# Kernel tuning notes

Hardware: AMD Instinct MI355X
Metric: run time of the kernel (lower is better)

Reference implementation:

```python
import jax, jax.numpy as jnp
import numpy as np

EPS = 1e-6
H, A, V = 4, 64, 64  # heads, attn_dim, hidden_dim


def layer_norm(x, w, b):
    mu = jnp.mean(x, axis=-1, keepdims=True)
    var = jnp.var(x, axis=-1, keepdims=True)
    return (x - mu) * jax.lax.rsqrt(var + EPS) * w + b


def setup_inputs() -> dict:
    key = jax.random.key(0)
    B, N, D = 4, 2048, 512
    lengths = np.array([2048, 1536, 1024, 1792], np.int32)
    offsets = np.concatenate([[0], np.cumsum(lengths)]).astype(np.int32)
    L = int(offsets[-1])  # 6400
    uvqk_out = (2 * V + 2 * A) * H  # 1024
    out_in = 2 * V * H + D          # concat([u, x, normed_attn])
    ks = jax.random.split(key, 4)
    return {
        "x": jax.random.normal(ks[0], (L, D), jnp.float32),
        "x_lengths": jnp.asarray(lengths),
        "x_offsets": jnp.asarray(offsets),
        "max_seq_len": N,
        "num_targets": jnp.asarray([32, 16, 8, 64], jnp.int32),
        "uvqk_weight": jax.random.normal(ks[1], (D, uvqk_out), jnp.float32) / np.float32(np.sqrt(D)),
        "uvqk_bias": jnp.zeros((uvqk_out,), jnp.float32),
        "input_norm_weight": jnp.ones((D,), jnp.float32),
        "input_norm_bias": jnp.zeros((D,), jnp.float32),
        "output_norm_weight": jnp.ones((V * H,), jnp.float32),
        "output_norm_bias": jnp.zeros((V * H,), jnp.float32),
        "output_weight": jax.random.normal(ks[2], (out_in, D), jnp.float32) / np.float32(np.sqrt(out_in)),
    }


def reference(x, x_lengths, x_offsets, max_seq_len, num_targets,
              uvqk_weight, uvqk_bias, input_norm_weight, input_norm_bias,
              output_norm_weight, output_norm_bias, output_weight):
    L, D = x.shape
    B = x_lengths.shape[0]
    N = int(max_seq_len)
    alpha = A ** -0.5

    # fused input layernorm + UVQK projection + silu
    nx = layer_norm(x, input_norm_weight, input_norm_bias)
    uvqk = jax.nn.silu(nx @ uvqk_weight + uvqk_bias)              # [L, (2V+2A)*H]
    u = uvqk[:, : V * H]                                          # [L, V*H]
    v = uvqk[:, V * H: 2 * V * H].reshape(L, H, V)
    q = uvqk[:, 2 * V * H: 2 * V * H + A * H].reshape(L, H, A)
    k = uvqk[:, 2 * V * H + A * H:].reshape(L, H, A)

    # jagged -> padded [B, N, ...]
    pos = jnp.arange(N)
    gather_idx = jnp.clip(x_offsets[:-1, None] + pos[None, :], 0, L - 1)  # [B,N]
    valid = pos[None, :] < x_lengths[:, None]                              # [B,N]
    qp = q[gather_idx] * valid[..., None, None]
    kp = k[gather_idx] * valid[..., None, None]
    vp = v[gather_idx] * valid[..., None, None]

    # target-aware causal mask: clamp ids at uih boundary; eye | dist>0
    max_ids = (x_lengths - num_targets)[:, None]        # [B,1]
    ids = jnp.minimum(pos[None, :], max_ids)            # [B,N]
    dist = ids[:, :, None] - ids[:, None, :]            # [B,N,N]
    mask = (dist > 0) | jnp.eye(N, dtype=bool)[None]
    mask = mask & valid[:, :, None] & valid[:, None, :]

    scores = jnp.einsum("bnha,bmha->bhnm", qp, kp) * alpha
    attn_w = jax.nn.silu(scores) * (1.0 / N)
    attn_w = attn_w * mask[:, None].astype(attn_w.dtype)
    attn_p = jnp.einsum("bhnm,bmhv->bnhv", attn_w, vp).reshape(B, N, H * V)

    # padded -> jagged
    tok = jnp.arange(L)
    b_of = jnp.searchsorted(x_offsets, tok, side="right") - 1
    p_of = tok - x_offsets[b_of]
    attn = attn_p[b_of, p_of]                            # [L, H*V]

    # output: norm(attn), concat [u, x, y], project, residual (dropout off / eval)
    y = layer_norm(attn, output_norm_weight, output_norm_bias)
    y = jnp.concatenate([u, x, y], axis=1)
    return x + y @ output_weight
```

## Files before the change

### kernel.cpp

```cpp
#include <hip/hip_runtime.h>
#include <math.h>

#define NSEQ 2048
#define PIT 72

typedef __attribute__((ext_vector_type(8))) short short8;
typedef __attribute__((ext_vector_type(4))) short short4v;
typedef __attribute__((ext_vector_type(4))) float f32x4;

__device__ __forceinline__ float silu_f(float z) {
    return z * __builtin_amdgcn_rcpf(1.f + __expf(-z));
}

__device__ __forceinline__ unsigned short f2bf(float f) {
    unsigned int u = __float_as_uint(f);
    u += 0x7fffu + ((u >> 16) & 1u);
    return (unsigned short)(u >> 16);
}

__device__ __forceinline__ unsigned short f2bf_fast(float f) {
    return (unsigned short)((__float_as_uint(f) + 0x8000u) >> 16);
}

__device__ __forceinline__ short8 scale8_pow2(short8 v, float s) {
    short8 r;
    #pragma unroll
    for (int i = 0; i < 8; i++) {
        float f = __uint_as_float(((unsigned int)(unsigned short)v[i]) << 16) * s;
        r[i] = (short)(unsigned short)(__float_as_uint(f) >> 16);
    }
    return r;
}

__global__ void __launch_bounds__(256) transpose_both(
    const float* __restrict__ W1, unsigned short* __restrict__ W1t,
    const float* __restrict__ W2, unsigned short* __restrict__ W2t)
{
    __shared__ float t[32][33];
    int id = blockIdx.x;
    const float* W; unsigned short* Wt; int R, C, bx, by;
    if (id < 512) { W = W1; Wt = W1t; R = 512;  C = 1024; bx = id & 31; by = id >> 5; }
    else { id -= 512; W = W2; Wt = W2t; R = 1024; C = 512;  bx = id & 15; by = id >> 4; }
    int tid = threadIdx.x;
    int tr = tid >> 5, tc = tid & 31;
    int r0 = by * 32, c0 = bx * 32;
    #pragma unroll
    for (int p = 0; p < 4; p++)
        t[tr + p * 8][tc] = W[(size_t)(r0 + tr + p * 8) * C + c0 + tc];
    __syncthreads();
    #pragma unroll
    for (int p = 0; p < 4; p++)
        Wt[(size_t)(c0 + tr + p * 8) * R + r0 + tc] = f2bf(t[tc][tr + p * 8]);
}

__global__ void __launch_bounds__(256) ln512_kernel(
    const float* __restrict__ x, const float* __restrict__ w,
    const float* __restrict__ b,
    unsigned short* __restrict__ nxb, unsigned short* __restrict__ A2)
{
    int tid = threadIdx.x, lane = tid & 63, wv = tid >> 6;
    int row = blockIdx.x * 4 + wv;
    int c = lane * 8;
    const float* xr = x + (size_t)row * 512 + c;
    float4 v0 = *(const float4*)xr;
    float4 v1 = *(const float4*)(xr + 4);
    float s  = v0.x + v0.y + v0.z + v0.w + v1.x + v1.y + v1.z + v1.w;
    float sq = v0.x * v0.x + v0.y * v0.y + v0.z * v0.z + v0.w * v0.w
             + v1.x * v1.x + v1.y * v1.y + v1.z * v1.z + v1.w * v1.w;
    #pragma unroll
    for (int o = 32; o > 0; o >>= 1) { s += __shfl_xor(s, o); sq += __shfl_xor(sq, o); }
    float mu = s * (1.f / 512.f);
    float var = sq * (1.f / 512.f) - mu * mu;
    float rs = rsqrtf(var + 1e-6f);
    float4 w0 = *(const float4*)(w + c), w1 = *(const float4*)(w + c + 4);
    float4 b0 = *(const float4*)(b + c), b1 = *(const float4*)(b + c + 4);
    ushort4 hn0, hn1, hx0, hx1;
    hn0.x = f2bf((v0.x - mu) * rs * w0.x + b0.x);
    hn0.y = f2bf((v0.y - mu) * rs * w0.y + b0.y);
    hn0.z = f2bf((v0.z - mu) * rs * w0.z + b0.z);
    hn0.w = f2bf((v0.w - mu) * rs * w0.w + b0.w);
    hn1.x = f2bf((v1.x - mu) * rs * w1.x + b1.x);
    hn1.y = f2bf((v1.y - mu) * rs * w1.y + b1.y);
    hn1.z = f2bf((v1.z - mu) * rs * w1.z + b1.z);
    hn1.w = f2bf((v1.w - mu) * rs * w1.w + b1.w);
    hx0.x = f2bf(v0.x); hx0.y = f2bf(v0.y); hx0.z = f2bf(v0.z); hx0.w = f2bf(v0.w);
    hx1.x = f2bf(v1.x); hx1.y = f2bf(v1.y); hx1.z = f2bf(v1.z); hx1.w = f2bf(v1.w);
    unsigned short* nr = nxb + (size_t)row * 512 + c;
    *(ushort4*)nr = hn0; *(ushort4*)(nr + 4) = hn1;
    unsigned short* ar = A2 + (size_t)row * 1024 + 256 + c;
    *(ushort4*)ar = hx0; *(ushort4*)(ar + 4) = hx1;
}

__global__ void __launch_bounds__(256) ln256_kernel(
    const float* __restrict__ a, const float* __restrict__ w,
    const float* __restrict__ b, unsigned short* __restrict__ A2)
{
    int tid = threadIdx.x, lane = tid & 63, wv = tid >> 6;
    int row = blockIdx.x * 4 + wv;
    int c = lane * 4;
    float4 v = *(const float4*)(a + (size_t)row * 256 + c);
    float s  = v.x + v.y + v.z + v.w;
    float sq = v.x * v.x + v.y * v.y + v.z * v.z + v.w * v.w;
    #pragma unroll
    for (int o = 32; o > 0; o >>= 1) { s += __shfl_xor(s, o); sq += __shfl_xor(sq, o); }
    float mu = s * (1.f / 256.f);
    float var = sq * (1.f / 256.f) - mu * mu;
    float rs = rsqrtf(var + 1e-6f);
    float4 w4 = *(const float4*)(w + c);
    float4 b4 = *(const float4*)(b + c);
    ushort4 h;
    h.x = f2bf((v.x - mu) * rs * w4.x + b4.x);
    h.y = f2bf((v.y - mu) * rs * w4.y + b4.y);
    h.z = f2bf((v.z - mu) * rs * w4.z + b4.z);
    h.w = f2bf((v.w - mu) * rs * w4.w + b4.w);
    *(ushort4*)(A2 + (size_t)row * 1024 + 768 + c) = h;
}

__global__ void __launch_bounds__(256) gemm1_mfma(
    const unsigned short* __restrict__ Ab, const unsigned short* __restrict__ Bt,
    const float* __restrict__ bias,
    unsigned short* __restrict__ A2, unsigned short* __restrict__ qkvb)
{
    constexpr int K = 512, KIT = K / 64;
    __shared__ unsigned short As[64 * PIT];
    __shared__ unsigned short Bs[128 * PIT];
    int tid = threadIdx.x, lane = tid & 63, w = tid >> 6;
    int wr = w >> 1, wc = w & 1;
    int nn = lane & 15, qd = lane >> 4;
    int bm = blockIdx.y * 64, bn = blockIdx.x * 128;
    int arow = tid >> 2, ac0 = (tid & 3) * 16;
    int brow = tid >> 1, bc0 = (tid & 1) * 32;
    const unsigned short* Ag = Ab + (size_t)(bm + arow) * K + ac0;
    const unsigned short* Bg = Bt + (size_t)(bn + brow) * K + bc0;

    short8 pa0 = *(const short8*)Ag, pa1 = *(const short8*)(Ag + 8);
    short8 pb0 = *(const short8*)Bg, pb1 = *(const short8*)(Bg + 8);
    short8 pb2 = *(const short8*)(Bg + 16), pb3 = *(const short8*)(Bg + 24);

    f32x4 acc[2][4];
    #pragma unroll
    for (int i = 0; i < 2; i++)
        #pragma unroll
        for (int j = 0; j < 4; j++) acc[i][j] = (f32x4){0.f, 0.f, 0.f, 0.f};

    for (int it = 0; it < KIT; ++it) {
        __syncthreads();
        *(short8*)&As[arow * PIT + ac0]     = pa0;
        *(short8*)&As[arow * PIT + ac0 + 8] = pa1;
        *(short8*)&Bs[brow * PIT + bc0]      = pb0;
        *(short8*)&Bs[brow * PIT + bc0 + 8]  = pb1;
        *(short8*)&Bs[brow * PIT + bc0 + 16] = pb2;
        *(short8*)&Bs[brow * PIT + bc0 + 24] = pb3;
        __syncthreads();
        if (it + 1 < KIT) {
            int k0 = (it + 1) * 64;
            pa0 = *(const short8*)(Ag + k0); pa1 = *(const short8*)(Ag + k0 + 8);
            pb0 = *(const short8*)(Bg + k0); pb1 = *(const short8*)(Bg + k0 + 8);
            pb2 = *(const short8*)(Bg + k0 + 16); pb3 = *(const short8*)(Bg + k0 + 24);
        }
        #pragma unroll
        for (int kk = 0; kk < 2; kk++) {
            short8 af[2], bf[4];
            #pragma unroll
            for (int i = 0; i < 2; i++)
                af[i] = *(const short8*)&As[(wr * 32 + i * 16 + nn) * PIT + kk * 32 + qd * 8];
            #pragma unroll
            for (int j = 0; j < 4; j++)
                bf[j] = *(const short8*)&Bs[(wc * 64 + j * 16 + nn) * PIT + kk * 32 + qd * 8];
            #pragma unroll
            for (int i = 0; i < 2; i++)
                #pragma unroll
                for (int j = 0; j < 4; j++)
                    acc[i][j] = __builtin_amdgcn_mfma_f32_16x16x32_bf16(af[i], bf[j], acc[i][j], 0, 0, 0);
        }
    }
    bool isU = (bn < 256);
    #pragma unroll
    for (int j = 0; j < 4; j++) {
        int col = bn + wc * 64 + j * 16 + nn;
        float bb = bias[col];
        #pragma unroll
        for (int i = 0; i < 2; i++) {
            int rbase = bm + wr * 32 + i * 16 + qd * 4;
            #pragma unroll
            for (int r = 0; r < 4; r++) {
                unsigned short hh = f2bf(silu_f(acc[i][j][r] + bb));
                if (isU) A2[(size_t)(rbase + r) * 1024 + col] = hh;
                else     qkvb[(size_t)(rbase + r) * 768 + col - 256] = hh;
            }
        }
    }
}

__global__ void __launch_bounds__(256) gemm2_mfma(
    const unsigned short* __restrict__ Ab, const unsigned short* __restrict__ Bt,
    const float* __restrict__ x, float* __restrict__ out)
{
    constexpr int K = 1024, KIT = K / 64;
    __shared__ unsigned short As[64 * PIT];
    __shared__ unsigned short Bs[128 * PIT];
    int tid = threadIdx.x, lane = tid & 63, w = tid >> 6;
    int wr = w >> 1, wc = w & 1;
    int nn = lane & 15, qd = lane >> 4;
    int bm = blockIdx.y * 64, bn = blockIdx.x * 128;
    int arow = tid >> 2, ac0 = (tid & 3) * 16;
    int brow = tid >> 1, bc0 = (tid & 1) * 32;
    const unsigned short* Ag = Ab + (size_t)(bm + arow) * K + ac0;
    const unsigned short* Bg = Bt + (size_t)(bn + brow) * K + bc0;

    short8 pa0 = *(const short8*)Ag, pa1 = *(const short8*)(Ag + 8);
    short8 pb0 = *(const short8*)Bg, pb1 = *(const short8*)(Bg + 8);
    short8 pb2 = *(const short8*)(Bg + 16), pb3 = *(const short8*)(Bg + 24);

    f32x4 acc[2][4];
    #pragma unroll
    for (int i = 0; i < 2; i++)
        #pragma unroll
        for (int j = 0; j < 4; j++) acc[i][j] = (f32x4){0.f, 0.f, 0.f, 0.f};

    for (int it = 0; it < KIT; ++it) {
        __syncthreads();
        *(short8*)&As[arow * PIT + ac0]     = pa0;
        *(short8*)&As[arow * PIT + ac0 + 8] = pa1;
        *(short8*)&Bs[brow * PIT + bc0]      = pb0;
        *(short8*)&Bs[brow * PIT + bc0 + 8]  = pb1;
        *(short8*)&Bs[brow * PIT + bc0 + 16] = pb2;
        *(short8*)&Bs[brow * PIT + bc0 + 24] = pb3;
        __syncthreads();
        if (it + 1 < KIT) {
            int k0 = (it + 1) * 64;
            pa0 = *(const short8*)(Ag + k0); pa1 = *(const short8*)(Ag + k0 + 8);
            pb0 = *(const short8*)(Bg + k0); pb1 = *(const short8*)(Bg + k0 + 8);
            pb2 = *(const short8*)(Bg + k0 + 16); pb3 = *(const short8*)(Bg + k0 + 24);
        }
        #pragma unroll
        for (int kk = 0; kk < 2; kk++) {
            short8 af[2], bf[4];
            #pragma unroll
            for (int i = 0; i < 2; i++)
                af[i] = *(const short8*)&As[(wr * 32 + i * 16 + nn) * PIT + kk * 32 + qd * 8];
            #pragma unroll
            for (int j = 0; j < 4; j++)
                bf[j] = *(const short8*)&Bs[(wc * 64 + j * 16 + nn) * PIT + kk * 32 + qd * 8];
            #pragma unroll
            for (int i = 0; i < 2; i++)
                #pragma unroll
                for (int j = 0; j < 4; j++)
                    acc[i][j] = __builtin_amdgcn_mfma_f32_16x16x32_bf16(af[i], bf[j], acc[i][j], 0, 0, 0);
        }
    }
    #pragma unroll
    for (int j = 0; j < 4; j++) {
        int col = bn + wc * 64 + j * 16 + nn;
        #pragma unroll
        for (int i = 0; i < 2; i++) {
            int rbase = bm + wr * 32 + i * 16 + qd * 4;
            #pragma unroll
            for (int r = 0; r < 4; r++) {
                size_t idx = (size_t)(rbase + r) * 512 + col;
                out[idx] = x[idx] + acc[i][j][r];
            }
        }
    }
}

__global__ void __launch_bounds__(256, 2) attn_mfma_kernel(
    const unsigned short* __restrict__ qkvb,
    const int* __restrict__ offsets,
    const int* __restrict__ lengths,
    const int* __restrict__ num_targets,
    float* __restrict__ attn)
{
    int id = blockIdx.x;
    int bh = id & 15;
    int xt = id >> 4;
    int b = bh >> 2, h = bh & 3;
    int len = lengths[b];
    int n0 = (31 - xt) * 64;
    if (n0 >= len) return;
    int m_hi = min(n0 + 63, len - 1);
    int off = offsets[b];
    int max_id = len - num_targets[b];
    int tid = threadIdx.x, lane = tid & 63, w = tid >> 6;
    int nn = lane & 15, qd = lane >> 4;

    __shared__ __align__(16) char smem[69632];
    unsigned short* Vt = (unsigned short*)(smem + w * 9216);
    float* Os = (float*)smem;

    short8 qf[4][2];
    #pragma unroll
    for (int g = 0; g < 4; g++) {
        int row = min(n0 + g * 16 + nn, len - 1);
        const unsigned short* base = qkvb + (size_t)(off + row) * 768 + 256 + h * 64;
        qf[g][0] = scale8_pow2(*(const short8*)(base + qd * 8), 0.125f);
        qf[g][1] = scale8_pow2(*(const short8*)(base + 32 + qd * 8), 0.125f);
    }

    f32x4 o_acc[4][4];
    #pragma unroll
    for (int t = 0; t < 4; t++)
        #pragma unroll
        for (int g = 0; g < 4; g++) o_acc[t][g] = (f32x4){0.f, 0.f, 0.f, 0.f};

    int fast_lim = min(n0, max_id);
    int r0 = (lane & 15) * 4, d0 = (lane >> 4) * 16;

    short8 kf[4][2], kn[4][2], vf[4][2];
    int m_first = w * 64;
    if (m_first <= m_hi) {
        #pragma unroll
        for (int s = 0; s < 4; s++) {
            int row = min(m_first + s * 16 + nn, len - 1);
            const unsigned short* kb = qkvb + (size_t)(off + row) * 768 + 512 + h * 64 + qd * 8;
            kf[s][0] = *(const short8*)kb;
            kf[s][1] = *(const short8*)(kb + 32);
        }
        #pragma unroll
        for (int j = 0; j < 4; j++) {
            int row = min(m_first + r0 + j, len - 1);
            const unsigned short* vb = qkvb + (size_t)(off + row) * 768 + h * 64 + d0;
            vf[j][0] = *(const short8*)vb;
            vf[j][1] = *(const short8*)(vb + 8);
        }
    }

    for (int m0 = m_first; m0 <= m_hi; m0 += 256) {
        #pragma unroll
        for (int dd = 0; dd < 16; dd++) {
            int hh = dd >> 3, e = dd & 7;
            short4v pk;
            pk[0] = vf[0][hh][e]; pk[1] = vf[1][hh][e];
            pk[2] = vf[2][hh][e]; pk[3] = vf[3][hh][e];
            *(short4v*)&Vt[(d0 + dd) * PIT + r0] = pk;
        }
        int mnext = m0 + 256;
        if (mnext <= m_hi) {
            #pragma unroll
            for (int j = 0; j < 4; j++) {
                int row = min(mnext + r0 + j, len - 1);
                const unsigned short* vb = qkvb + (size_t)(off + row) * 768 + h * 64 + d0;
                vf[j][0] = *(const short8*)vb;
                vf[j][1] = *(const short8*)(vb + 8);
            }
            #pragma unroll
            for (int s = 0; s < 4; s++) {
                int row = min(mnext + s * 16 + nn, len - 1);
                const unsigned short* kb = qkvb + (size_t)(off + row) * 768 + 512 + h * 64 + qd * 8;
                kn[s][0] = *(const short8*)kb;
                kn[s][1] = *(const short8*)(kb + 32);
            }
        }
        bool fastp = (m0 + 63 < fast_lim);
        #pragma unroll
        for (int s = 0; s < 4; s++) {
            f32x4 st[4];
            __builtin_amdgcn_s_setprio(1);
            #pragma unroll
            for (int g = 0; g < 4; g++) {
                st[g] = (f32x4){0.f, 0.f, 0.f, 0.f};
                st[g] = __builtin_amdgcn_mfma_f32_16x16x32_bf16(kf[s][0], qf[g][0], st[g], 0, 0, 0);
                st[g] = __builtin_amdgcn_mfma_f32_16x16x32_bf16(kf[s][1], qf[g][1], st[g], 0, 0, 0);
            }
            __builtin_amdgcn_s_setprio(0);
            short4v bop[4];
            if (fastp) {
                #pragma unroll
                for (int g = 0; g < 4; g++)
                    #pragma unroll
                    for (int r = 0; r < 4; r++)
                        bop[g][r] = (short)f2bf_fast(silu_f(st[g][r]));
            } else {
                #pragma unroll
                for (int g = 0; g < 4; g++) {
                    int nc_ = n0 + g * 16 + nn;
                    int id_ = min(nc_, max_id);
                    #pragma unroll
                    for (int r = 0; r < 4; r++) {
                        int mcol = m0 + s * 16 + qd * 4 + r;
                        bool ok = (mcol < id_) || (mcol == nc_);
                        bop[g][r] = (short)f2bf_fast(ok ? silu_f(st[g][r]) : 0.f);
                    }
                }
            }
            __builtin_amdgcn_s_setprio(1);
            #pragma unroll
            for (int t = 0; t < 4; t++) {
                short4v aop = *(const short4v*)&Vt[(t * 16 + nn) * PIT + s * 16 + qd * 4];
                #pragma unroll
                for (int g = 0; g < 4; g++)
                    o_acc[t][g] = __builtin_amdgcn_mfma_f32_16x16x16bf16_1k(aop, bop[g], o_acc[t][g], 0, 0, 0);
            }
            __builtin_amdgcn_s_setprio(0);
        }
        if (mnext <= m_hi) {
            #pragma unroll
            for (int s = 0; s < 4; s++) { kf[s][0] = kn[s][0]; kf[s][1] = kn[s][1]; }
        }
    }

    __syncthreads();
    const float invN = 1.f / (float)NSEQ;
    float* Ow = Os + w * 4352;
    #pragma unroll
    for (int t = 0; t < 4; t++)
        #pragma unroll
        for (int g = 0; g < 4; g++) {
            f32x4 v = o_acc[t][g] * invN;
            *(f32x4*)&Ow[(g * 16 + nn) * 68 + t * 16 + qd * 4] = v;
        }
    __syncthreads();
    int rr = tid >> 2, cs = (tid & 3) * 16;
    if (n0 + rr < len) {
        float* dst = attn + (size_t)(off + n0 + rr) * 256 + h * 64 + cs;
        #pragma unroll
        for (int q4 = 0; q4 < 4; q4++) {
            f32x4 v = (f32x4){0.f, 0.f, 0.f, 0.f};
            #pragma unroll
            for (int w2 = 0; w2 < 4; w2++)
                v += *(const f32x4*)&Os[w2 * 4352 + rr * 68 + cs + q4 * 4];
            *(f32x4*)(dst + q4 * 4) = v;
        }
    }
}

extern "C" void kernel_launch(void* const* d_in, const int* in_sizes, int n_in,
                              void* d_out, int out_size, void* d_ws, size_t ws_size,
                              hipStream_t stream)
{
    const float* x          = (const float*)d_in[0];
    const int*   x_lengths  = (const int*)d_in[1];
    const int*   x_offsets  = (const int*)d_in[2];
    const int*   num_targets = (const int*)d_in[4];
    const float* uvqk_w     = (const float*)d_in[5];
    const float* uvqk_b     = (const float*)d_in[6];
    const float* in_w       = (const float*)d_in[7];
    const float* in_b       = (const float*)d_in[8];
    const float* out_w      = (const float*)d_in[9];
    const float* out_b      = (const float*)d_in[10];
    const float* Wo         = (const float*)d_in[11];
    float* out = (float*)d_out;

    int L = in_sizes[0] / 512;
    int B = in_sizes[1];

    char* ws = (char*)d_ws;
    size_t o = 0;
    float* attn = (float*)(ws + o);          o += (size_t)L * 256 * 4;
    unsigned short* nxb  = (unsigned short*)(ws + o); o += (size_t)L * 512 * 2;
    unsigned short* A2   = (unsigned short*)(ws + o); o += (size_t)L * 1024 * 2;
    unsigned short* qkvb = (unsigned short*)(ws + o); o += (size_t)L * 768 * 2;
    unsigned short* W1t  = (unsigned short*)(ws + o); o += (size_t)1024 * 512 * 2;
    unsigned short* W2t  = (unsigned short*)(ws + o); o += (size_t)512 * 1024 * 2;

    transpose_both<<<dim3(1024), 256, 0, stream>>>(uvqk_w, W1t, Wo, W2t);

    ln512_kernel<<<L / 4, 256, 0, stream>>>(x, in_w, in_b, nxb, A2);

    dim3 g1(1024 / 128, L / 64);
    gemm1_mfma<<<g1, 256, 0, stream>>>(nxb, W1t, uvqk_b, A2, qkvb);

    attn_mfma_kernel<<<dim3(512), 256, 0, stream>>>(qkvb, x_offsets, x_lengths, num_targets, attn);

    ln256_kernel<<<L / 4, 256, 0, stream>>>(attn, out_w, out_b, A2);

    dim3 g3(512 / 128, L / 64);
    gemm2_mfma<<<g3, 256, 0, stream>>>(A2, W2t, x, out);
}
```

Measured before the change: 165.0 us.

## Fuse output layernorm into GEMM2 prologue and merge prep kernels

Merges the weight transpose and input layernorm into a single prep kernel, and computes the output layernorm of attention inside the output GEMM, staging the normalized rows in shared memory for the last K chunk. This removes two kernel launches and a global write/read of the normalized attention. In exchange each row's layernorm is recomputed once per column block, and the extra LDS buffer and register array may reduce GEMM occupancy.

```diff
diff --git a/kernel.cpp b/kernel.cpp
--- a/kernel.cpp
+++ b/kernel.cpp
@@ -3,6 +3,7 @@
 
 #define NSEQ 2048
 #define PIT 72
+#define YP 264
 
 typedef __attribute__((ext_vector_type(8))) short short8;
 typedef __attribute__((ext_vector_type(4))) short short4v;
@@ -32,34 +33,33 @@
     return r;
 }
 
-__global__ void __launch_bounds__(256) transpose_both(
+__global__ void __launch_bounds__(256) prep_kernel(
     const float* __restrict__ W1, unsigned short* __restrict__ W1t,
-    const float* __restrict__ W2, unsigned short* __restrict__ W2t)
+    const float* __restrict__ W2, unsigned short* __restrict__ W2t,
+    const float* __restrict__ x, const float* __restrict__ inw,
+    const float* __restrict__ inb,
+    unsigned short* __restrict__ nxb, unsigned short* __restrict__ A2)
 {
     __shared__ float t[32][33];
     int id = blockIdx.x;
-    const float* W; unsigned short* Wt; int R, C, bx, by;
-    if (id < 512) { W = W1; Wt = W1t; R = 512;  C = 1024; bx = id & 31; by = id >> 5; }
-    else { id -= 512; W = W2; Wt = W2t; R = 1024; C = 512;  bx = id & 15; by = id >> 4; }
     int tid = threadIdx.x;
-    int tr = tid >> 5, tc = tid & 31;
-    int r0 = by * 32, c0 = bx * 32;
-    #pragma unroll
-    for (int p = 0; p < 4; p++)
-        t[tr + p * 8][tc] = W[(size_t)(r0 + tr + p * 8) * C + c0 + tc];
-    __syncthreads();
-    #pragma unroll
-    for (int p = 0; p < 4; p++)
-        Wt[(size_t)(c0 + tr + p * 8) * R + r0 + tc] = f2bf(t[tc][tr + p * 8]);
-}
-
-__global__ void __launch_bounds__(256) ln512_kernel(
-    const float* __restrict__ x, const float* __restrict__ w,
-    const float* __restrict__ b,
-    unsigned short* __restrict__ nxb, unsigned short* __restrict__ A2)
-{
-    int tid = threadIdx.x, lane = tid & 63, wv = tid >> 6;
-    int row = blockIdx.x * 4 + wv;
+    if (id < 1024) {
+        const float* W; unsigned short* Wt; int R, C, bx, by;
+        if (id < 512) { W = W1; Wt = W1t; R = 512;  C = 1024; bx = id & 31; by = id >> 5; }
+        else { int i2 = id - 512; W = W2; Wt = W2t; R = 1024; C = 512; bx = i2 & 15; by = i2 >> 4; }
+        int tr = tid >> 5, tc = tid & 31;
+        int r0 = by * 32, c0 = bx * 32;
+        #pragma unroll
+        for (int p = 0; p < 4; p++)
+            t[tr + p * 8][tc] = W[(size_t)(r0 + tr + p * 8) * C + c0 + tc];
+        __syncthreads();
+        #pragma unroll
+        for (int p = 0; p < 4; p++)
+            Wt[(size_t)(c0 + tr + p * 8) * R + r0 + tc] = f2bf(t[tc][tr + p * 8]);
+        return;
+    }
+    int lane = tid & 63, wv = tid >> 6;
+    int row = (id - 1024) * 4 + wv;
     int c = lane * 8;
     const float* xr = x + (size_t)row * 512 + c;
     float4 v0 = *(const float4*)xr;
@@ -72,8 +72,8 @@
     float mu = s * (1.f / 512.f);
     float var = sq * (1.f / 512.f) - mu * mu;
     float rs = rsqrtf(var + 1e-6f);
-    float4 w0 = *(const float4*)(w + c), w1 = *(const float4*)(w + c + 4);
-    float4 b0 = *(const float4*)(b + c), b1 = *(const float4*)(b + c + 4);
+    float4 w0 = *(const float4*)(inw + c), w1 = *(const float4*)(inw + c + 4);
+    float4 b0 = *(const float4*)(inb + c), b1 = *(const float4*)(inb + c + 4);
     ushort4 hn0, hn1, hx0, hx1;
     hn0.x = f2bf((v0.x - mu) * rs * w0.x + b0.x);
     hn0.y = f2bf((v0.y - mu) * rs * w0.y + b0.y);
@@ -89,31 +89,6 @@
     *(ushort4*)nr = hn0; *(ushort4*)(nr + 4) = hn1;
     unsigned short* ar = A2 + (size_t)row * 1024 + 256 + c;
     *(ushort4*)ar = hx0; *(ushort4*)(ar + 4) = hx1;
-}
-
-__global__ void __launch_bounds__(256) ln256_kernel(
-    const float* __restrict__ a, const float* __restrict__ w,
-    const float* __restrict__ b, unsigned short* __restrict__ A2)
-{
-    int tid = threadIdx.x, lane = tid & 63, wv = tid >> 6;
-    int row = blockIdx.x * 4 + wv;
-    int c = lane * 4;
-    float4 v = *(const float4*)(a + (size_t)row * 256 + c);
-    float s  = v.x + v.y + v.z + v.w;
-    float sq = v.x * v.x + v.y * v.y + v.z * v.z + v.w * v.w;
-    #pragma unroll
-    for (int o = 32; o > 0; o >>= 1) { s += __shfl_xor(s, o); sq += __shfl_xor(sq, o); }
-    float mu = s * (1.f / 256.f);
-    float var = sq * (1.f / 256.f) - mu * mu;
-    float rs = rsqrtf(var + 1e-6f);
-    float4 w4 = *(const float4*)(w + c);
-    float4 b4 = *(const float4*)(b + c);
-    ushort4 h;
-    h.x = f2bf((v.x - mu) * rs * w4.x + b4.x);
-    h.y = f2bf((v.y - mu) * rs * w4.y + b4.y);
-    h.z = f2bf((v.z - mu) * rs * w4.z + b4.z);
-    h.w = f2bf((v.w - mu) * rs * w4.w + b4.w);
-    *(ushort4*)(A2 + (size_t)row * 1024 + 768 + c) = h;
 }
 
 __global__ void __launch_bounds__(256) gemm1_mfma(
@@ -192,13 +167,16 @@
     }
 }
 
-__global__ void __launch_bounds__(256) gemm2_mfma(
+__global__ void __launch_bounds__(256) gemm2_ln_mfma(
     const unsigned short* __restrict__ Ab, const unsigned short* __restrict__ Bt,
+    const float* __restrict__ attn, const float* __restrict__ ow,
+    const float* __restrict__ ob,
     const float* __restrict__ x, float* __restrict__ out)
 {
     constexpr int K = 1024, KIT = K / 64;
     __shared__ unsigned short As[64 * PIT];
     __shared__ unsigned short Bs[128 * PIT];
+    __shared__ __align__(16) unsigned short Ys[64 * YP];
     int tid = threadIdx.x, lane = tid & 63, w = tid >> 6;
     int wr = w >> 1, wc = w & 1;
     int nn = lane & 15, qd = lane >> 4;
@@ -211,6 +189,38 @@
     short8 pa0 = *(const short8*)Ag, pa1 = *(const short8*)(Ag + 8);
     short8 pb0 = *(const short8*)Bg, pb1 = *(const short8*)(Bg + 8);
     short8 pb2 = *(const short8*)(Bg + 16), pb3 = *(const short8*)(Bg + 24);
+
+    {
+        int rrow = tid >> 2, qq = tid & 3;
+        const float* ar = attn + (size_t)(bm + rrow) * 256 + qq * 64;
+        float vx[64];
+        float s = 0.f, sq = 0.f;
+        #pragma unroll
+        for (int i = 0; i < 16; i++) {
+            float4 v4 = *(const float4*)(ar + i * 4);
+            vx[4 * i] = v4.x; vx[4 * i + 1] = v4.y; vx[4 * i + 2] = v4.z; vx[4 * i + 3] = v4.w;
+            s += v4.x + v4.y + v4.z + v4.w;
+            sq += v4.x * v4.x + v4.y * v4.y + v4.z * v4.z + v4.w * v4.w;
+        }
+        s += __shfl_xor(s, 1); sq += __shfl_xor(sq, 1);
+        s += __shfl_xor(s, 2); sq += __shfl_xor(sq, 2);
+        float mu = s * (1.f / 256.f);
+        float var = sq * (1.f / 256.f) - mu * mu;
+        float rs = rsqrtf(var + 1e-6f);
+        unsigned short* yr = &Ys[rrow * YP + qq * 64];
+        #pragma unroll
+        for (int i = 0; i < 16; i++) {
+            float4 w4 = *(const float4*)(ow + qq * 64 + i * 4);
+            float4 b4 = *(const float4*)(ob + qq * 64 + i * 4);
+            ushort4 h;
+            h.x = f2bf((vx[4 * i]     - mu) * rs * w4.x + b4.x);
+            h.y = f2bf((vx[4 * i + 1] - mu) * rs * w4.y + b4.y);
+            h.z = f2bf((vx[4 * i + 2] - mu) * rs * w4.z + b4.z);
+            h.w = f2bf((vx[4 * i + 3] - mu) * rs * w4.w + b4.w);
+            *(ushort4*)(yr + i * 4) = h;
+        }
+    }
+    __syncthreads();
 
     f32x4 acc[2][4];
     #pragma unroll
@@ -229,7 +239,12 @@
         __syncthreads();
         if (it + 1 < KIT) {
             int k0 = (it + 1) * 64;
-            pa0 = *(const short8*)(Ag + k0); pa1 = *(const short8*)(Ag + k0 + 8);
+            if (k0 < 768) {
+                pa0 = *(const short8*)(Ag + k0); pa1 = *(const short8*)(Ag + k0 + 8);
+            } else {
+                const unsigned short* ys = &Ys[arow * YP + (k0 - 768) + ac0];
+                pa0 = *(const short8*)ys; pa1 = *(const short8*)(ys + 8);
+            }
             pb0 = *(const short8*)(Bg + k0); pb1 = *(const short8*)(Bg + k0 + 8);
             pb2 = *(const short8*)(Bg + k0 + 16); pb3 = *(const short8*)(Bg + k0 + 24);
         }
@@ -442,7 +457,6 @@
     float* out = (float*)d_out;
 
     int L = in_sizes[0] / 512;
-    int B = in_sizes[1];
 
     char* ws = (char*)d_ws;
     size_t o = 0;
@@ -453,17 +467,14 @@
     unsigned short* W1t  = (unsigned short*)(ws + o); o += (size_t)1024 * 512 * 2;
     unsigned short* W2t  = (unsigned short*)(ws + o); o += (size_t)512 * 1024 * 2;
 
-    transpose_both<<<dim3(1024), 256, 0, stream>>>(uvqk_w, W1t, Wo, W2t);
-
-    ln512_kernel<<<L / 4, 256, 0, stream>>>(x, in_w, in_b, nxb, A2);
+    prep_kernel<<<dim3(1024 + L / 4), 256, 0, stream>>>(
+        uvqk_w, W1t, Wo, W2t, x, in_w, in_b, nxb, A2);
 
     dim3 g1(1024 / 128, L / 64);
     gemm1_mfma<<<g1, 256, 0, stream>>>(nxb, W1t, uvqk_b, A2, qkvb);
 
     attn_mfma_kernel<<<dim3(512), 256, 0, stream>>>(qkvb, x_offsets, x_lengths, num_targets, attn);
 
-    ln256_kernel<<<L / 4, 256, 0, stream>>>(attn, out_w, out_b, A2);
-
     dim3 g3(512 / 128, L / 64);
-    gemm2_mfma<<<g3, 256, 0, stream>>>(A2, W2t, x, out);
-}
+    gemm2_ln_mfma<<<g3, 256, 0, stream>>>(A2, W2t, attn, out_w, out_b, x, out);
+}
```

Result: slower. 182.0 us (+10.3%).
